# Performance work log

Hardware: AMD Instinct MI355X
Metric: run time of the kernel (lower is better)

Reference implementation:

```python
import jax, jax.numpy as jnp
import numpy as np
import math

B, NH, T, D = 4, 4, 512, 256
MULT = 128
N = MULT * D // NH  # 8192
MAXLEN = 512
THETA = 2 ** 16
SCALE = N ** -0.5


def _cos_sin():
    # freqs with pairwise quantization: 1/theta**(floor(i/2)*2/N)/(2*pi)
    idx = np.arange(N, dtype=np.float32)
    freqs = 1.0 / THETA ** (np.floor(idx / 2.0) * 2.0 / N) / (2.0 * math.pi)
    phases = np.arange(MAXLEN, dtype=np.float32)[:, None] * freqs[None, :]
    angles = (phases % 1.0) * (2.0 * math.pi)
    return jnp.asarray(np.cos(angles), jnp.float32), jnp.asarray(np.sin(angles), jnp.float32)


def setup_inputs() -> dict:
    key = jax.random.key(0)
    k1, k2, k3 = jax.random.split(key, 3)
    Q = jax.random.uniform(k1, (B, NH, T, N), dtype=jnp.float32)  # post-ReLU sparse acts
    V = jax.random.normal(k2, (B, 1, T, D), dtype=jnp.float32)
    state = jax.random.normal(k3, (B, NH, N, D), dtype=jnp.float32) * 0.02
    cos, sin = _cos_sin()
    return {"Q": Q, "V": V, "state": state, "cos": cos, "sin": sin}


def _rope(v, cos, sin):
    # rotate-half with interleaved pairs: (-v_odd, v_even) interleaved back
    v_even = v[..., ::2]
    v_odd = v[..., 1::2]
    v_rot = jnp.stack([-v_odd, v_even], axis=-1).reshape(v.shape)
    return v * cos + v_rot * sin


def reference(Q, V, state, cos, sin):
    # cos/sin: (MAXLEN, N) -> slice first T positions, broadcast over (B, NH)
    QR = _rope(Q, cos[:T], sin[:T])                      # (B, NH, T, N)
    scores = jnp.matmul(QR, jnp.swapaxes(QR, -2, -1)) * SCALE  # (B, NH, T, T)
    causal = jnp.tril(jnp.ones((T, T), dtype=bool), k=-1)      # strictly lower
    scores = jnp.where(causal, scores, 0.0)
    output = jnp.matmul(scores, V)                       # V (B,1,T,D) broadcasts -> (B,NH,T,D)
    output = output + jnp.matmul(QR, state)              # recurrent state contribution
    chunk_state = jnp.matmul(jnp.swapaxes(QR, -2, -1), V) * SCALE  # (B, NH, N, D)
    new_state = state + chunk_state
    return output, new_state
```

## Files before the change

### kernel.cpp

```cpp
#include <hip/hip_runtime.h>
#include <stdint.h>

#define B_ 4
#define NH_ 4
#define T_ 512
#define D_ 256
#define N_ 8192
#define NHEAD 16
#define SCALE_ 0.011048543456039806f

typedef __attribute__((ext_vector_type(8))) short bf16x8;
typedef __attribute__((ext_vector_type(4))) float f32x4;

__device__ __forceinline__ unsigned short f2bf(float x) {
  union { float f; unsigned u; } v; v.f = x;
  unsigned r = v.u + 0x7fffu + ((v.u >> 16) & 1u);
  return (unsigned short)(r >> 16);
}

__device__ __forceinline__ void async16(const void* g, void* l) {
  __builtin_amdgcn_global_load_lds(
      (const __attribute__((address_space(1))) unsigned int*)g,
      (__attribute__((address_space(3))) unsigned int*)l,
      16, 0, 0);
}

__device__ __forceinline__ void stage_direct(const unsigned short* __restrict__ g,
                                             int ld, unsigned short* lds, int t) {
  const int row = t >> 2, c8 = (t & 3) * 8;
  async16(g + (size_t)row * ld + c8, lds + row * 32 + c8);
  async16(g + (size_t)(row + 64) * ld + c8, lds + (row + 64) * 32 + c8);
}

__device__ __forceinline__ void stage_trans_bf16(const unsigned short* __restrict__ g,
                                                 int ld, unsigned short* lds, int t) {
  const int mn = t & 127, ks = (t >> 7) * 16;
  __attribute__((aligned(16))) unsigned short u[16];
  #pragma unroll
  for (int i = 0; i < 16; i++) u[i] = g[(size_t)(ks + i) * ld + mn];
  *(uint4*)(lds + mn * 40 + ks)     = *(const uint4*)u;
  *(uint4*)(lds + mn * 40 + ks + 8) = *(const uint4*)(u + 8);
}

__device__ __forceinline__ void stage_trans_f32(const float* __restrict__ g,
                                                int ld, unsigned short* lds, int t) {
  const int mn = t & 127, ks = (t >> 7) * 16;
  float f[16];
  #pragma unroll
  for (int i = 0; i < 16; i++) f[i] = g[(size_t)(ks + i) * ld + mn];
  __attribute__((aligned(16))) unsigned short u[16];
  #pragma unroll
  for (int i = 0; i < 16; i++) u[i] = f2bf(f[i]);
  *(uint4*)(lds + mn * 40 + ks)     = *(const uint4*)u;
  *(uint4*)(lds + mn * 40 + ks + 8) = *(const uint4*)(u + 8);
}

__device__ __forceinline__ void mfma_step(const unsigned short* as, int lda,
                                          const unsigned short* bs, int ldb,
                                          int wr, int wc, int lane, f32x4 acc[4][4]) {
  const int q8 = (lane >> 4) * 8, rl = lane & 15;
  bf16x8 a[4], b[4];
  #pragma unroll
  for (int i = 0; i < 4; i++)
    a[i] = *(const bf16x8*)(as + (wr * 64 + i * 16 + rl) * lda + q8);
  #pragma unroll
  for (int j = 0; j < 4; j++)
    b[j] = *(const bf16x8*)(bs + (wc * 64 + j * 16 + rl) * ldb + q8);
  #pragma unroll
  for (int i = 0; i < 4; i++)
    #pragma unroll
    for (int j = 0; j < 4; j++)
      acc[i][j] = __builtin_amdgcn_mfma_f32_16x16x32_bf16(a[i], b[j], acc[i][j], 0, 0, 0);
}

__global__ __launch_bounds__(256) void rope_kernel(
    const float* __restrict__ Q, const float* __restrict__ Cos,
    const float* __restrict__ Sin, unsigned short* __restrict__ QR)
{
  size_t i8 = ((size_t)blockIdx.x * 256 + threadIdx.x) * 8;
  int t = (int)((i8 >> 13) & (T_ - 1));
  int n = (int)(i8 & (N_ - 1));
  const float4 q0 = *(const float4*)(Q + i8);
  const float4 q1 = *(const float4*)(Q + i8 + 4);
  const float* cp = Cos + (size_t)t * N_ + n;
  const float* sp = Sin + (size_t)t * N_ + n;
  float4 c0 = *(const float4*)cp, c1 = *(const float4*)(cp + 4);
  float4 s0 = *(const float4*)sp, s1 = *(const float4*)(sp + 4);
  __attribute__((aligned(16))) unsigned short u[8];
  u[0] = f2bf(q0.x * c0.x - q0.y * s0.x);
  u[1] = f2bf(q0.y * c0.y + q0.x * s0.y);
  u[2] = f2bf(q0.z * c0.z - q0.w * s0.z);
  u[3] = f2bf(q0.w * c0.w + q0.z * s0.w);
  u[4] = f2bf(q1.x * c1.x - q1.y * s1.x);
  u[5] = f2bf(q1.y * c1.y + q1.x * s1.y);
  u[6] = f2bf(q1.z * c1.z - q1.w * s1.z);
  u[7] = f2bf(q1.w * c1.w + q1.z * s1.w);
  *(uint4*)(QR + i8) = *(const uint4*)u;
}

#define NB_SC 160
#define NB_OP 128
#define NB_NS 2048
#define OUT_STATE_OFF ((size_t)NHEAD * T_ * D_)

__global__ __launch_bounds__(256) void mega_kernel(
    const unsigned short* __restrict__ QR, const float* __restrict__ V,
    const float* __restrict__ state, unsigned short* __restrict__ Sc,
    float* __restrict__ Out)
{
  __shared__ unsigned short as[128 * 40];
  __shared__ unsigned short bs[128 * 40];
  const int blk = blockIdx.x, t = threadIdx.x;
  const int lane = t & 63, w = t >> 6, wr = w >> 1, wc = w & 1;
  const int q4 = (lane >> 4) * 4, rl = lane & 15;
  f32x4 acc[4][4];
  #pragma unroll
  for (int i = 0; i < 4; i++)
    #pragma unroll
    for (int j = 0; j < 4; j++) acc[i][j] = (f32x4){0.f, 0.f, 0.f, 0.f};

  if (blk < NB_SC) {
    static const int TI[10] = {0,1,1,2,2,2,3,3,3,3};
    static const int TJ[10] = {0,0,1,0,1,2,0,1,2,3};
    const int head = blk / 10, ti = TI[blk % 10], tj = TJ[blk % 10];
    const unsigned short* A  = QR + (size_t)head * T_ * N_ + (size_t)ti * 128 * N_;
    const unsigned short* Bp = QR + (size_t)head * T_ * N_ + (size_t)tj * 128 * N_;
    for (int k0 = 0; k0 < N_; k0 += 32) {
      stage_direct(A + k0, N_, as, t);
      stage_direct(Bp + k0, N_, bs, t);
      __syncthreads();
      mfma_step(as, 32, bs, 32, wr, wc, lane, acc);
      __syncthreads();
    }
    unsigned short* op = Sc + (size_t)head * T_ * T_;
    const bool diag = (ti == tj);
    #pragma unroll
    for (int i = 0; i < 4; i++)
      #pragma unroll
      for (int j = 0; j < 4; j++)
        #pragma unroll
        for (int r = 0; r < 4; r++) {
          int gi = ti * 128 + wr * 64 + i * 16 + q4 + r;
          int gj = tj * 128 + wc * 64 + j * 16 + rl;
          float v = acc[i][j][r] * SCALE_;
          if (diag && gj >= gi) v = 0.f;
          op[(size_t)gi * T_ + gj] = f2bf(v);
        }
  } else if (blk < NB_SC + NB_OP) {
    const int idx = blk - NB_SC;
    const int head = idx >> 3, mt = (idx & 7) >> 1, nt = idx & 1;
    const unsigned short* A = QR + (size_t)head * T_ * N_ + (size_t)mt * 128 * N_;
    const float* Bp = state + (size_t)head * N_ * D_ + nt * 128;
    for (int k0 = 0; k0 < N_; k0 += 32) {
      stage_direct(A + k0, N_, as, t);
      stage_trans_f32(Bp + (size_t)k0 * D_, D_, bs, t);
      __syncthreads();
      mfma_step(as, 32, bs, 40, wr, wc, lane, acc);
      __syncthreads();
    }
    float* op = Out + (size_t)head * T_ * D_;
    #pragma unroll
    for (int i = 0; i < 4; i++)
      #pragma unroll
      for (int j = 0; j < 4; j++)
        #pragma unroll
        for (int r = 0; r < 4; r++) {
          int gi = mt * 128 + wr * 64 + i * 16 + q4 + r;
          int gj = nt * 128 + wc * 64 + j * 16 + rl;
          op[(size_t)gi * D_ + gj] = acc[i][j][r];
        }
  } else if (blk < NB_SC + NB_OP + NB_NS) {
    const int idx = blk - (NB_SC + NB_OP);
    const int head = idx >> 7, mt = (idx & 127) >> 1, nt = idx & 1;
    const unsigned short* Asrc = QR + (size_t)head * T_ * N_ + mt * 128;
    const float* Bp = V + (size_t)(head >> 2) * T_ * D_ + nt * 128;
    for (int k0 = 0; k0 < T_; k0 += 32) {
      stage_trans_bf16(Asrc + (size_t)k0 * N_, N_, as, t);
      stage_trans_f32(Bp + (size_t)k0 * D_, D_, bs, t);
      __syncthreads();
      mfma_step(as, 40, bs, 40, wr, wc, lane, acc);
      __syncthreads();
    }
    const float* st = state + (size_t)head * N_ * D_;
    float* op = Out + OUT_STATE_OFF + (size_t)head * N_ * D_;
    #pragma unroll
    for (int i = 0; i < 4; i++)
      #pragma unroll
      for (int j = 0; j < 4; j++)
        #pragma unroll
        for (int r = 0; r < 4; r++) {
          int gm = mt * 128 + wr * 64 + i * 16 + q4 + r;
          int gd = nt * 128 + wc * 64 + j * 16 + rl;
          size_t off = (size_t)gm * D_ + gd;
          op[off] = st[off] + SCALE_ * acc[i][j][r];
        }
  } else {
    static const int ZI[6] = {0,0,0,1,1,2};
    static const int ZJ[6] = {1,2,3,2,3,3};
    const int idx = blk - (NB_SC + NB_OP + NB_NS);
    const int head = idx / 6, ti = ZI[idx % 6], tj = ZJ[idx % 6];
    unsigned short* op = Sc + (size_t)head * T_ * T_;
    const uint4 z = make_uint4(0u, 0u, 0u, 0u);
    #pragma unroll
    for (int v = 0; v < 8; v++) {
      int e = v * 256 + t;
      int r = e >> 4, c = (e & 15) * 8;
      *(uint4*)(op + (size_t)(ti * 128 + r) * T_ + tj * 128 + c) = z;
    }
  }
}

__global__ __launch_bounds__(256) void final_kernel(
    const unsigned short* __restrict__ Sc, const float* __restrict__ V,
    float* __restrict__ Out)
{
  __shared__ unsigned short as[128 * 32];
  __shared__ unsigned short bs[128 * 40];
  const int blk = blockIdx.x, t = threadIdx.x;
  const int lane = t & 63, w = t >> 6, wr = w >> 1, wc = w & 1;
  const int q4 = (lane >> 4) * 4, rl = lane & 15;
  const int head = blk >> 3, mt = (blk & 7) >> 1, nt = blk & 1;
  const unsigned short* A = Sc + (size_t)head * T_ * T_ + (size_t)mt * 128 * T_;
  const float* Bp = V + (size_t)(head >> 2) * T_ * D_ + nt * 128;
  f32x4 acc[4][4];
  #pragma unroll
  for (int i = 0; i < 4; i++)
    #pragma unroll
    for (int j = 0; j < 4; j++) acc[i][j] = (f32x4){0.f, 0.f, 0.f, 0.f};
  for (int k0 = 0; k0 < T_; k0 += 32) {
    stage_direct(A + k0, T_, as, t);
    stage_trans_f32(Bp + (size_t)k0 * D_, D_, bs, t);
    __syncthreads();
    mfma_step(as, 32, bs, 40, wr, wc, lane, acc);
    __syncthreads();
  }
  float* op = Out + (size_t)head * T_ * D_;
  #pragma unroll
  for (int i = 0; i < 4; i++)
    #pragma unroll
    for (int j = 0; j < 4; j++)
      #pragma unroll
      for (int r = 0; r < 4; r++) {
        int gi = mt * 128 + wr * 64 + i * 16 + q4 + r;
        int gj = nt * 128 + wc * 64 + j * 16 + rl;
        size_t off = (size_t)gi * D_ + gj;
        op[off] = op[off] + acc[i][j][r];
      }
}

extern "C" void kernel_launch(void* const* d_in, const int* in_sizes, int n_in,
                              void* d_out, int out_size, void* d_ws, size_t ws_size,
                              hipStream_t stream) {
  const float* Q     = (const float*)d_in[0];
  const float* V     = (const float*)d_in[1];
  const float* state = (const float*)d_in[2];
  const float* Cos   = (const float*)d_in[3];
  const float* Sin   = (const float*)d_in[4];
  float* out = (float*)d_out;

  unsigned short* QR = (unsigned short*)d_ws;
  unsigned short* Sc = QR + (size_t)NHEAD * T_ * N_;

  rope_kernel<<<dim3(32768), dim3(256), 0, stream>>>(Q, Cos, Sin, QR);
  mega_kernel<<<dim3(NB_SC + NB_OP + NB_NS + 96), dim3(256), 0, stream>>>(QR, V, state, Sc, out);
  final_kernel<<<dim3(128), dim3(256), 0, stream>>>(Sc, V, out);
}
```

Measured before the change: 864.8 us.

## Split-K long reductions with atomics, compute RoPE on the fly, swizzle LDS tiles

The N=8192 reductions (scores and QR·state) are split four ways across more blocks and combined with float atomics into zeroed buffers. The final kernel is also split-K, and the mask and scale are now applied while staging fp32 scores. RoPE recomputes cos/sin in-kernel from the position and frequency formula instead of reading the cos/sin tables. LDS tiles are XOR-swizzled to reduce bank conflicts. The aim is better occupancy on the long-K tiles and less memory traffic. The cost is atomic traffic, extra memsets and small float differences from approximate sin/cos and nondeterministic summation order.

```diff
diff --git a/kernel.cpp b/kernel.cpp
--- a/kernel.cpp
+++ b/kernel.cpp
@@ -1,13 +1,12 @@
 #include <hip/hip_runtime.h>
 #include <stdint.h>
 
-#define B_ 4
-#define NH_ 4
 #define T_ 512
 #define D_ 256
 #define N_ 8192
 #define NHEAD 16
 #define SCALE_ 0.011048543456039806f
+#define INV2PI 0.15915493667125702f
 
 typedef __attribute__((ext_vector_type(8))) short bf16x8;
 typedef __attribute__((ext_vector_type(4))) float f32x4;
@@ -27,9 +26,12 @@
 
 __device__ __forceinline__ void stage_direct(const unsigned short* __restrict__ g,
                                              int ld, unsigned short* lds, int t) {
-  const int row = t >> 2, c8 = (t & 3) * 8;
-  async16(g + (size_t)row * ld + c8, lds + row * 32 + c8);
-  async16(g + (size_t)(row + 64) * ld + c8, lds + (row + 64) * 32 + c8);
+  const int row = t >> 2, b = t & 3;
+  const int g1 = (b ^ ((row >> 1) & 3)) * 8;
+  async16(g + (size_t)row * ld + g1, lds + row * 32 + b * 8);
+  const int row2 = row + 64;
+  const int g2 = (b ^ ((row2 >> 1) & 3)) * 8;
+  async16(g + (size_t)row2 * ld + g2, lds + row2 * 32 + b * 8);
 }
 
 __device__ __forceinline__ void stage_trans_bf16(const unsigned short* __restrict__ g,
@@ -55,17 +57,45 @@
   *(uint4*)(lds + mn * 40 + ks + 8) = *(const uint4*)(u + 8);
 }
 
-__device__ __forceinline__ void mfma_step(const unsigned short* as, int lda,
-                                          const unsigned short* bs, int ldb,
+__device__ __forceinline__ void stage_sc(const float* __restrict__ g, int gi0, int gk0,
+                                         unsigned short* lds, int t) {
+  const int row = t >> 2, c8 = (t & 3) * 8;
+  #pragma unroll
+  for (int rr = 0; rr < 2; rr++) {
+    const int r = row + rr * 64;
+    const float* p = g + (size_t)r * T_ + c8;
+    float4 x = *(const float4*)p, y = *(const float4*)(p + 4);
+    float f[8] = {x.x, x.y, x.z, x.w, y.x, y.y, y.z, y.w};
+    const int gi = gi0 + r;
+    __attribute__((aligned(16))) unsigned short u[8];
+    #pragma unroll
+    for (int e = 0; e < 8; e++) {
+      float v = ((gk0 + c8 + e) < gi) ? f[e] * SCALE_ : 0.f;
+      u[e] = f2bf(v);
+    }
+    *(uint4*)(lds + r * 40 + c8) = *(const uint4*)u;
+  }
+}
+
+template<bool SWA, bool SWB>
+__device__ __forceinline__ void mfma_step(const unsigned short* as, const unsigned short* bs,
                                           int wr, int wc, int lane, f32x4 acc[4][4]) {
-  const int q8 = (lane >> 4) * 8, rl = lane & 15;
+  const int j8 = lane >> 4, rl = lane & 15;
+  const int swz = (j8 ^ ((rl >> 1) & 3)) * 8;
+  const int pad = j8 * 8;
   bf16x8 a[4], b[4];
   #pragma unroll
-  for (int i = 0; i < 4; i++)
-    a[i] = *(const bf16x8*)(as + (wr * 64 + i * 16 + rl) * lda + q8);
-  #pragma unroll
-  for (int j = 0; j < 4; j++)
-    b[j] = *(const bf16x8*)(bs + (wc * 64 + j * 16 + rl) * ldb + q8);
+  for (int i = 0; i < 4; i++) {
+    int r = wr * 64 + i * 16 + rl;
+    a[i] = SWA ? *(const bf16x8*)(as + r * 32 + swz)
+               : *(const bf16x8*)(as + r * 40 + pad);
+  }
+  #pragma unroll
+  for (int j = 0; j < 4; j++) {
+    int r = wc * 64 + j * 16 + rl;
+    b[j] = SWB ? *(const bf16x8*)(bs + r * 32 + swz)
+               : *(const bf16x8*)(bs + r * 40 + pad);
+  }
   #pragma unroll
   for (int i = 0; i < 4; i++)
     #pragma unroll
@@ -74,38 +104,39 @@
 }
 
 __global__ __launch_bounds__(256) void rope_kernel(
-    const float* __restrict__ Q, const float* __restrict__ Cos,
-    const float* __restrict__ Sin, unsigned short* __restrict__ QR)
+    const float* __restrict__ Q, unsigned short* __restrict__ QR)
 {
   size_t i8 = ((size_t)blockIdx.x * 256 + threadIdx.x) * 8;
-  int t = (int)((i8 >> 13) & (T_ - 1));
-  int n = (int)(i8 & (N_ - 1));
-  const float4 q0 = *(const float4*)(Q + i8);
-  const float4 q1 = *(const float4*)(Q + i8 + 4);
-  const float* cp = Cos + (size_t)t * N_ + n;
-  const float* sp = Sin + (size_t)t * N_ + n;
-  float4 c0 = *(const float4*)cp, c1 = *(const float4*)(cp + 4);
-  float4 s0 = *(const float4*)sp, s1 = *(const float4*)(sp + 4);
+  const int t = (int)((i8 >> 13) & (T_ - 1));
+  const int n = (int)(i8 & (N_ - 1));
+  float q[8];
+  *(float4*)q       = *(const float4*)(Q + i8);
+  *(float4*)(q + 4) = *(const float4*)(Q + i8 + 4);
+  const float ft = (float)t;
   __attribute__((aligned(16))) unsigned short u[8];
-  u[0] = f2bf(q0.x * c0.x - q0.y * s0.x);
-  u[1] = f2bf(q0.y * c0.y + q0.x * s0.y);
-  u[2] = f2bf(q0.z * c0.z - q0.w * s0.z);
-  u[3] = f2bf(q0.w * c0.w + q0.z * s0.w);
-  u[4] = f2bf(q1.x * c1.x - q1.y * s1.x);
-  u[5] = f2bf(q1.y * c1.y + q1.x * s1.y);
-  u[6] = f2bf(q1.z * c1.z - q1.w * s1.z);
-  u[7] = f2bf(q1.w * c1.w + q1.z * s1.w);
+  #pragma unroll
+  for (int p = 0; p < 4; p++) {
+    const int h = (n >> 1) + p;
+    float f = exp2f((float)h * (-1.0f / 256.0f)) * INV2PI;
+    float r = ft * f;
+    r = r - floorf(r);
+    float c = __builtin_amdgcn_cosf(r);
+    float s = __builtin_amdgcn_sinf(r);
+    float ev = q[2 * p], od = q[2 * p + 1];
+    u[2 * p]     = f2bf(ev * c - od * s);
+    u[2 * p + 1] = f2bf(od * c + ev * s);
+  }
   *(uint4*)(QR + i8) = *(const uint4*)u;
 }
 
-#define NB_SC 160
-#define NB_OP 128
+#define NB_SC 640
+#define NB_OP 512
 #define NB_NS 2048
 #define OUT_STATE_OFF ((size_t)NHEAD * T_ * D_)
 
 __global__ __launch_bounds__(256) void mega_kernel(
     const unsigned short* __restrict__ QR, const float* __restrict__ V,
-    const float* __restrict__ state, unsigned short* __restrict__ Sc,
+    const float* __restrict__ state, float* __restrict__ ScF,
     float* __restrict__ Out)
 {
   __shared__ unsigned short as[128 * 40];
@@ -122,18 +153,19 @@
   if (blk < NB_SC) {
     static const int TI[10] = {0,1,1,2,2,2,3,3,3,3};
     static const int TJ[10] = {0,0,1,0,1,2,0,1,2,3};
-    const int head = blk / 10, ti = TI[blk % 10], tj = TJ[blk % 10];
+    const int tile = blk >> 2, split = blk & 3;
+    const int head = tile / 10, ti = TI[tile % 10], tj = TJ[tile % 10];
     const unsigned short* A  = QR + (size_t)head * T_ * N_ + (size_t)ti * 128 * N_;
     const unsigned short* Bp = QR + (size_t)head * T_ * N_ + (size_t)tj * 128 * N_;
-    for (int k0 = 0; k0 < N_; k0 += 32) {
+    const int kbeg = split * 2048, kend = kbeg + 2048;
+    for (int k0 = kbeg; k0 < kend; k0 += 32) {
       stage_direct(A + k0, N_, as, t);
       stage_direct(Bp + k0, N_, bs, t);
       __syncthreads();
-      mfma_step(as, 32, bs, 32, wr, wc, lane, acc);
-      __syncthreads();
-    }
-    unsigned short* op = Sc + (size_t)head * T_ * T_;
-    const bool diag = (ti == tj);
+      mfma_step<true, true>(as, bs, wr, wc, lane, acc);
+      __syncthreads();
+    }
+    float* op = ScF + (size_t)head * T_ * T_;
     #pragma unroll
     for (int i = 0; i < 4; i++)
       #pragma unroll
@@ -142,20 +174,20 @@
         for (int r = 0; r < 4; r++) {
           int gi = ti * 128 + wr * 64 + i * 16 + q4 + r;
           int gj = tj * 128 + wc * 64 + j * 16 + rl;
-          float v = acc[i][j][r] * SCALE_;
-          if (diag && gj >= gi) v = 0.f;
-          op[(size_t)gi * T_ + gj] = f2bf(v);
+          unsafeAtomicAdd(op + (size_t)gi * T_ + gj, acc[i][j][r]);
         }
   } else if (blk < NB_SC + NB_OP) {
     const int idx = blk - NB_SC;
-    const int head = idx >> 3, mt = (idx & 7) >> 1, nt = idx & 1;
+    const int tile = idx >> 2, split = idx & 3;
+    const int head = tile >> 3, mt = (tile & 7) >> 1, nt = tile & 1;
     const unsigned short* A = QR + (size_t)head * T_ * N_ + (size_t)mt * 128 * N_;
     const float* Bp = state + (size_t)head * N_ * D_ + nt * 128;
-    for (int k0 = 0; k0 < N_; k0 += 32) {
+    const int kbeg = split * 2048, kend = kbeg + 2048;
+    for (int k0 = kbeg; k0 < kend; k0 += 32) {
       stage_direct(A + k0, N_, as, t);
       stage_trans_f32(Bp + (size_t)k0 * D_, D_, bs, t);
       __syncthreads();
-      mfma_step(as, 32, bs, 40, wr, wc, lane, acc);
+      mfma_step<true, false>(as, bs, wr, wc, lane, acc);
       __syncthreads();
     }
     float* op = Out + (size_t)head * T_ * D_;
@@ -167,9 +199,9 @@
         for (int r = 0; r < 4; r++) {
           int gi = mt * 128 + wr * 64 + i * 16 + q4 + r;
           int gj = nt * 128 + wc * 64 + j * 16 + rl;
-          op[(size_t)gi * D_ + gj] = acc[i][j][r];
+          unsafeAtomicAdd(op + (size_t)gi * D_ + gj, acc[i][j][r]);
         }
-  } else if (blk < NB_SC + NB_OP + NB_NS) {
+  } else {
     const int idx = blk - (NB_SC + NB_OP);
     const int head = idx >> 7, mt = (idx & 127) >> 1, nt = idx & 1;
     const unsigned short* Asrc = QR + (size_t)head * T_ * N_ + mt * 128;
@@ -178,7 +210,7 @@
       stage_trans_bf16(Asrc + (size_t)k0 * N_, N_, as, t);
       stage_trans_f32(Bp + (size_t)k0 * D_, D_, bs, t);
       __syncthreads();
-      mfma_step(as, 40, bs, 40, wr, wc, lane, acc);
+      mfma_step<false, false>(as, bs, wr, wc, lane, acc);
       __syncthreads();
     }
     const float* st = state + (size_t)head * N_ * D_;
@@ -194,44 +226,33 @@
           size_t off = (size_t)gm * D_ + gd;
           op[off] = st[off] + SCALE_ * acc[i][j][r];
         }
-  } else {
-    static const int ZI[6] = {0,0,0,1,1,2};
-    static const int ZJ[6] = {1,2,3,2,3,3};
-    const int idx = blk - (NB_SC + NB_OP + NB_NS);
-    const int head = idx / 6, ti = ZI[idx % 6], tj = ZJ[idx % 6];
-    unsigned short* op = Sc + (size_t)head * T_ * T_;
-    const uint4 z = make_uint4(0u, 0u, 0u, 0u);
-    #pragma unroll
-    for (int v = 0; v < 8; v++) {
-      int e = v * 256 + t;
-      int r = e >> 4, c = (e & 15) * 8;
-      *(uint4*)(op + (size_t)(ti * 128 + r) * T_ + tj * 128 + c) = z;
-    }
   }
 }
 
 __global__ __launch_bounds__(256) void final_kernel(
-    const unsigned short* __restrict__ Sc, const float* __restrict__ V,
+    const float* __restrict__ ScF, const float* __restrict__ V,
     float* __restrict__ Out)
 {
-  __shared__ unsigned short as[128 * 32];
+  __shared__ unsigned short as[128 * 40];
   __shared__ unsigned short bs[128 * 40];
   const int blk = blockIdx.x, t = threadIdx.x;
   const int lane = t & 63, w = t >> 6, wr = w >> 1, wc = w & 1;
   const int q4 = (lane >> 4) * 4, rl = lane & 15;
-  const int head = blk >> 3, mt = (blk & 7) >> 1, nt = blk & 1;
-  const unsigned short* A = Sc + (size_t)head * T_ * T_ + (size_t)mt * 128 * T_;
+  const int tile = blk >> 1, split = blk & 1;
+  const int head = tile >> 3, mt = (tile & 7) >> 1, nt = tile & 1;
+  const float* A = ScF + (size_t)head * T_ * T_ + (size_t)mt * 128 * T_;
   const float* Bp = V + (size_t)(head >> 2) * T_ * D_ + nt * 128;
   f32x4 acc[4][4];
   #pragma unroll
   for (int i = 0; i < 4; i++)
     #pragma unroll
     for (int j = 0; j < 4; j++) acc[i][j] = (f32x4){0.f, 0.f, 0.f, 0.f};
-  for (int k0 = 0; k0 < T_; k0 += 32) {
-    stage_direct(A + k0, T_, as, t);
+  const int kbeg = split * 256, kend = kbeg + 256;
+  for (int k0 = kbeg; k0 < kend; k0 += 32) {
+    stage_sc(A + k0, mt * 128, k0, as, t);
     stage_trans_f32(Bp + (size_t)k0 * D_, D_, bs, t);
     __syncthreads();
-    mfma_step(as, 32, bs, 40, wr, wc, lane, acc);
+    mfma_step<false, false>(as, bs, wr, wc, lane, acc);
     __syncthreads();
   }
   float* op = Out + (size_t)head * T_ * D_;
@@ -243,8 +264,7 @@
       for (int r = 0; r < 4; r++) {
         int gi = mt * 128 + wr * 64 + i * 16 + q4 + r;
         int gj = nt * 128 + wc * 64 + j * 16 + rl;
-        size_t off = (size_t)gi * D_ + gj;
-        op[off] = op[off] + acc[i][j][r];
+        unsafeAtomicAdd(op + (size_t)gi * D_ + gj, acc[i][j][r]);
       }
 }
 
@@ -254,14 +274,14 @@
   const float* Q     = (const float*)d_in[0];
   const float* V     = (const float*)d_in[1];
   const float* state = (const float*)d_in[2];
-  const float* Cos   = (const float*)d_in[3];
-  const float* Sin   = (const float*)d_in[4];
   float* out = (float*)d_out;
 
   unsigned short* QR = (unsigned short*)d_ws;
-  unsigned short* Sc = QR + (size_t)NHEAD * T_ * N_;
-
-  rope_kernel<<<dim3(32768), dim3(256), 0, stream>>>(Q, Cos, Sin, QR);
-  mega_kernel<<<dim3(NB_SC + NB_OP + NB_NS + 96), dim3(256), 0, stream>>>(QR, V, state, Sc, out);
-  final_kernel<<<dim3(128), dim3(256), 0, stream>>>(Sc, V, out);
-}
+  float* ScF = (float*)((char*)d_ws + (size_t)NHEAD * T_ * N_ * 2);
+
+  hipMemsetAsync(ScF, 0, (size_t)NHEAD * T_ * T_ * 4, stream);
+  hipMemsetAsync(out, 0, (size_t)NHEAD * T_ * D_ * 4, stream);
+  rope_kernel<<<dim3(32768), dim3(256), 0, stream>>>(Q, QR);
+  mega_kernel<<<dim3(NB_SC + NB_OP + NB_NS), dim3(256), 0, stream>>>(QR, V, state, ScF, out);
+  final_kernel<<<dim3(256), dim3(256), 0, stream>>>(ScF, V, out);
+}
```

Result: faster. 796.6 us (-7.9%).
